# Kernel optimization log

Hardware: AMD Instinct MI355X
Metric: run time of the kernel (lower is better)

## Reference

```python
import jax, jax.numpy as jnp
import numpy as np

DIM = 256
HEADS = 8
PS = 8  # patch/window size
EPS = 1e-5


def _ln(x, g, b):
    m = x.mean(-1, keepdims=True)
    v = x.var(-1, keepdims=True)
    return (x - m) / jnp.sqrt(v + EPS) * g + b


def setup_inputs() -> dict:
    key = jax.random.key(0)
    ks = jax.random.split(key, 10)
    B, C, H, W = 4, DIM, 256, 256
    s = 0.02
    return {
        "y_lf": jax.random.normal(ks[0], (B, C, H, W), jnp.float32),
        "y_hf": jax.random.normal(ks[1], (B, C, H, W), jnp.float32),
        "g_lf": jnp.ones((C,), jnp.float32),
        "b_lf": jnp.zeros((C,), jnp.float32),
        "g_hf": jnp.ones((C,), jnp.float32),
        "b_hf": jnp.zeros((C,), jnp.float32),
        "Wq": jax.random.normal(ks[2], (C, C), jnp.float32) * s,
        "bq": jnp.zeros((C,), jnp.float32),
        "Wk": jax.random.normal(ks[3], (C, C), jnp.float32) * s,
        "bk": jnp.zeros((C,), jnp.float32),
        "Wv": jax.random.normal(ks[4], (C, C), jnp.float32) * s,
        "bv": jnp.zeros((C,), jnp.float32),
        "Wo": jax.random.normal(ks[5], (C, C), jnp.float32) * s,
        "bo": jnp.zeros((C,), jnp.float32),
    }


def reference(y_lf, y_hf, g_lf, b_lf, g_hf, b_hf, Wq, bq, Wk, bk, Wv, bv, Wo, bo):
    B, C, H, W = y_lf.shape
    ps = PS
    hd = C // HEADS
    nH, nW = H // ps, W // ps

    def win_tokens(x):
        # (B,C,H,W) -> (B*nH*nW, ps*ps, C)
        x = x.reshape(B, C, nH, ps, nW, ps)
        return x.transpose(0, 2, 4, 3, 5, 1).reshape(-1, ps * ps, C)

    lf = win_tokens(y_lf)
    hf = win_tokens(y_hf)  # residual + V source (un-normalized, as in torch code)

    q = _ln(lf, g_lf, b_lf) @ Wq.T + bq
    k = _ln(hf, g_hf, b_hf) @ Wk.T + bk
    v = hf @ Wv.T + bv

    BW, L, _ = q.shape
    q = q.reshape(BW, L, HEADS, hd)
    k = k.reshape(BW, L, HEADS, hd)
    v = v.reshape(BW, L, HEADS, hd)

    scale = 1.0 / np.sqrt(hd).astype(np.float32)
    scores = jnp.einsum('bqhd,bkhd->bhqk', q, k) * scale
    attn = jax.nn.softmax(scores, axis=-1)
    o = jnp.einsum('bhqk,bkhd->bqhd', attn, v).reshape(BW, L, C)
    o = o @ Wo.T + bo + hf  # out_proj + residual

    # window_reverse: (B*nH*nW, ps*ps, C) -> (B,C,H,W)
    o = o.reshape(B, nH, nW, ps, ps, C)
    o = o.transpose(0, 5, 1, 3, 2, 4).reshape(B, C, H, W)
    return o
```

## Files before the change

kernel.cpp:

```cpp
#include <hip/hip_runtime.h>

typedef float  f4     __attribute__((ext_vector_type(4)));
typedef float  f32x4  __attribute__((ext_vector_type(4)));
typedef short  short8 __attribute__((ext_vector_type(8)));
typedef __bf16 bf16x8 __attribute__((ext_vector_type(8)));
typedef int    int4v  __attribute__((ext_vector_type(4)));
typedef unsigned short us4 __attribute__((ext_vector_type(4)));

__device__ __forceinline__ unsigned short f2bf(float f) {
    unsigned int u = __builtin_bit_cast(unsigned int, f);
    u += 0x7FFFu + ((u >> 16) & 1u);
    return (unsigned short)(u >> 16);
}
__device__ __forceinline__ float bf2f(unsigned short h) {
    unsigned int u = ((unsigned int)h) << 16;
    return __builtin_bit_cast(float, u);
}
__device__ __forceinline__ f32x4 mfma_bf16(short8 a, short8 b, f32x4 c) {
    return __builtin_amdgcn_mfma_f32_16x16x32_bf16(
        __builtin_bit_cast(bf16x8, a), __builtin_bit_cast(bf16x8, b), c, 0, 0, 0);
}
__device__ __forceinline__ int cvt_pk_bf16(float lo, float hi) {
    int d;
    asm volatile("v_cvt_pk_bf16_f32 %0, %1, %2" : "=v"(d) : "v"(lo), "v"(hi));
    return d;
}
__device__ __forceinline__ int bperm(int addr, int src) {
    return __builtin_amdgcn_ds_bpermute(addr, src);
}

__global__ void pcaf_precvt(const float* __restrict__ Wq, const float* __restrict__ bq,
                            const float* __restrict__ Wk, const float* __restrict__ bk,
                            const float* __restrict__ Wv, const float* __restrict__ Wo,
                            const float* __restrict__ g_lf, const float* __restrict__ b_lf,
                            const float* __restrict__ g_hf, const float* __restrict__ b_hf,
                            void* __restrict__ ws) {
    const int mat  = blockIdx.x >> 8;
    const int row  = blockIdx.x & 255;
    const int lane = threadIdx.x;
    const float* W = (mat == 0) ? Wq : (mat == 1) ? Wk : (mat == 2) ? Wv : Wo;
    f4 w = *(const f4*)(W + row * 256 + lane * 4);
    f4 wp = w;
    if (mat < 2) {
        const float* g = mat ? g_hf : g_lf;
        f4 gg = *(const f4*)(g + lane * 4);
        wp = w * gg;
    }
    us4 u;
    u[0] = f2bf(wp[0]); u[1] = f2bf(wp[1]); u[2] = f2bf(wp[2]); u[3] = f2bf(wp[3]);
    {
        const int ct   = row >> 4;
        const int l15r = row & 15;
        const int k_   = lane >> 3;
        const int g_   = (lane >> 1) & 3;
        const int e4   = (lane & 1) * 4;
        unsigned short* dst = (unsigned short*)ws + mat * 65536 +
                              (((ct * 8 + k_) * 64) + g_ * 16 + l15r) * 8 + e4;
        *(us4*)dst = u;
    }
    if (mat < 2) {
        const float* b = mat ? b_hf : b_lf;
        f4 bb = *(const f4*)(b + lane * 4);
        float rsum = wp[0] + wp[1] + wp[2] + wp[3];
        float cb   = bb[0] * w[0] + bb[1] * w[1] + bb[2] * w[2] + bb[3] * w[3];
        #pragma unroll
        for (int d = 1; d < 64; d <<= 1) {
            rsum += __shfl_xor(rsum, d);
            cb   += __shfl_xor(cb, d);
        }
        if (lane == 0) {
            float* cons = (float*)((char*)ws + 524288);
            cons[mat * 512 + row]       = rsum;
            cons[mat * 512 + 256 + row] = cb + (mat ? bk[row] : bq[row]);
        }
    }
}

constexpr int RS  = 528;
constexpr int HWC = 65536;
constexpr int Wd  = 256;
constexpr int OA  = 0;
constexpr int OB  = 67584;
constexpr int OS  = 135168;

struct AccW { f32x4 a[4][2]; };

__device__ __forceinline__ AccW gemmW(const char* base,
                                      const unsigned short* __restrict__ Wbw,
                                      int lane, int g, int l15) {
    AccW r;
    f32x4 z = {0.f, 0.f, 0.f, 0.f};
    #pragma unroll
    for (int m = 0; m < 4; ++m) { r.a[m][0] = z; r.a[m][1] = z; }
    #pragma unroll
    for (int half = 0; half < 2; ++half) {
        short8 w0[4], w1[4];
        #pragma unroll
        for (int k = 0; k < 4; ++k) {
            w0[k] = *(const short8*)(Wbw + (half * 4 + k) * 512 + lane * 8);
            w1[k] = *(const short8*)(Wbw + 4096 + (half * 4 + k) * 512 + lane * 8);
        }
        #pragma unroll
        for (int k = 0; k < 4; ++k) {
            #pragma unroll
            for (int m = 0; m < 4; ++m) {
                short8 am = *(const short8*)(base + (16 * m + l15) * RS +
                                             ((half * 4 + k) * 32 + g * 8) * 2);
                r.a[m][0] = mfma_bf16(am, w0[k], r.a[m][0]);
                r.a[m][1] = mfma_bf16(am, w1[k], r.a[m][1]);
            }
        }
    }
    return r;
}

__global__ __attribute__((amdgpu_flat_work_group_size(1024, 1024)))
void pcaf8_kernel(
    const float* __restrict__ y_lf, const float* __restrict__ y_hf,
    const float* __restrict__ bv, const float* __restrict__ bo,
    const void* __restrict__ ws, float* __restrict__ out)
{
    __shared__ __align__(16) char sm[137216];

    const unsigned short* wsq = (const unsigned short*)ws;
    const unsigned short* wsk = wsq + 65536;
    const unsigned short* wsv = wsq + 131072;
    const unsigned short* wso = wsq + 196608;
    const float* cons = (const float*)((const char*)ws + 524288);

    const int tid = threadIdx.x;
    const int bid = blockIdx.x;
    const int wi  = ((bid & 7) << 8) | (bid >> 3);
    const int bb  = wi >> 9;
    const int nh  = (wi >> 4) & 31;
    const int nwp = wi & 15;
    const long pair_base = (long)bb * 256 * HWC + (long)(nh * 8) * Wd + nwp * 16;

    const int wave = tid >> 6;
    const int win  = wave >> 3;
    const int head = wave & 7;
    const int lane = tid & 63;
    const int g    = lane >> 4;
    const int l15  = lane & 15;
    const int c0   = 32 * head + l15;
    const int ro   = win * 64;

    {
        f4 lv[8], hv[8];
        #pragma unroll
        for (int it = 0; it < 4; ++it) {
            int q2  = it * 1024 + tid;
            int c2  = q2 >> 5;
            int ph  = (q2 >> 2) & 7;
            int pw4 = (q2 & 3) * 4;
            long go = pair_base + (long)(2 * c2) * HWC + ph * Wd + pw4;
            lv[2 * it]     = *(const f4*)(y_lf + go);
            lv[2 * it + 1] = *(const f4*)(y_lf + go + HWC);
            hv[2 * it]     = *(const f4*)(y_hf + go);
            hv[2 * it + 1] = *(const f4*)(y_hf + go + HWC);
        }
        #pragma unroll
        for (int it = 0; it < 4; ++it) {
            int q2  = it * 1024 + tid;
            int c2  = q2 >> 5;
            int ph  = (q2 >> 2) & 7;
            int pw4 = (q2 & 3) * 4;
            int tok0 = (pw4 >> 3) * 64 + ph * 8 + (pw4 & 7);
            #pragma unroll
            for (int j = 0; j < 4; ++j) {
                unsigned int lvv = (unsigned int)f2bf(lv[2 * it][j]) | ((unsigned int)f2bf(lv[2 * it + 1][j]) << 16);
                unsigned int hvv = (unsigned int)f2bf(hv[2 * it][j]) | ((unsigned int)f2bf(hv[2 * it + 1][j]) << 16);
                *(unsigned int*)(sm + OA + (tok0 + j) * RS + c2 * 4) = lvv;
                *(unsigned int*)(sm + OB + (tok0 + j) * RS + c2 * 4) = hvv;
            }
        }
    }
    __syncthreads();

    {
        const int t = tid >> 3, j = tid & 7;
        #pragma unroll
        for (int pass = 0; pass < 2; ++pass) {
            const int base = pass ? OB : OA;
            float sum = 0.f, ss = 0.f;
            #pragma unroll
            for (int r = 0; r < 4; ++r) {
                short8 raw = *(const short8*)(sm + base + t * RS + (j * 32 + r * 8) * 2);
                #pragma unroll
                for (int e = 0; e < 8; ++e) { float f = bf2f((unsigned short)raw[e]); sum += f; ss += f * f; }
            }
            sum += __shfl_xor(sum, 1); ss += __shfl_xor(ss, 1);
            sum += __shfl_xor(sum, 2); ss += __shfl_xor(ss, 2);
            sum += __shfl_xor(sum, 4); ss += __shfl_xor(ss, 4);
            float mean = sum * (1.f / 256.f);
            float rstd = rsqrtf(ss * (1.f / 256.f) - mean * mean + 1e-5f);
            if (j == 0) {
                float* S = (float*)(sm + OS);
                S[pass * 256 + t]       = mean;
                S[pass * 256 + 128 + t] = rstd;
            }
        }
    }

    AccW qacc = gemmW(sm + OA + ro * RS, wsq + head * 8192, lane, g, l15);

    unsigned int resp[4][2][2];
    #pragma unroll
    for (int m = 0; m < 4; ++m)
        #pragma unroll
        for (int n = 0; n < 2; ++n)
            #pragma unroll
            for (int jh = 0; jh < 2; ++jh) {
                unsigned int lo = *(const unsigned short*)(sm + OB + (ro + 16 * m + 4 * g + 2 * jh) * RS + (c0 + 16 * n) * 2);
                unsigned int hi = *(const unsigned short*)(sm + OB + (ro + 16 * m + 4 * g + 2 * jh + 1) * RS + (c0 + 16 * n) * 2);
                resp[m][n][jh] = lo | (hi << 16);
            }

    int vp[4][2][2];
    {
        AccW vacc = gemmW(sm + OB + ro * RS, wsv + head * 8192, lane, g, l15);
        float bv0 = bv[c0], bv1 = bv[c0 + 16];
        #pragma unroll
        for (int m = 0; m < 4; ++m) {
            vp[m][0][0] = cvt_pk_bf16(vacc.a[m][0][0] + bv0, vacc.a[m][0][1] + bv0);
            vp[m][0][1] = cvt_pk_bf16(vacc.a[m][0][2] + bv0, vacc.a[m][0][3] + bv0);
            vp[m][1][0] = cvt_pk_bf16(vacc.a[m][1][0] + bv1, vacc.a[m][1][1] + bv1);
            vp[m][1][1] = cvt_pk_bf16(vacc.a[m][1][2] + bv1, vacc.a[m][1][3] + bv1);
        }
    }
    __syncthreads();

    {
        const float* S = (const float*)(sm + OS);
        const float SCALE = 0.17677669529663687f;
        float rs0 = cons[c0], rs1 = cons[c0 + 16];
        float cb0 = cons[256 + c0], cb1 = cons[256 + c0 + 16];
        #pragma unroll
        for (int m = 0; m < 4; ++m)
            #pragma unroll
            for (int i = 0; i < 4; ++i) {
                int t = ro + 16 * m + 4 * g + i;
                float mean = S[t], rstd = S[128 + t];
                float v0 = (rstd * (qacc.a[m][0][i] - mean * rs0) + cb0) * SCALE;
                float v1 = (rstd * (qacc.a[m][1][i] - mean * rs1) + cb1) * SCALE;
                *(unsigned short*)(sm + OA + t * RS + c0 * 2)        = f2bf(v0);
                *(unsigned short*)(sm + OA + t * RS + (c0 + 16) * 2) = f2bf(v1);
            }
    }

    AccW kacc = gemmW(sm + OB + ro * RS, wsk + head * 8192, lane, g, l15);
    __syncthreads();

    {
        const float* S = (const float*)(sm + OS);
        float rs0 = cons[512 + c0], rs1 = cons[512 + c0 + 16];
        float cb0 = cons[768 + c0], cb1 = cons[768 + c0 + 16];
        #pragma unroll
        for (int m = 0; m < 4; ++m)
            #pragma unroll
            for (int i = 0; i < 4; ++i) {
                int t = ro + 16 * m + 4 * g + i;
                float mean = S[256 + t], rstd = S[384 + t];
                float v0 = rstd * (kacc.a[m][0][i] - mean * rs0) + cb0;
                float v1 = rstd * (kacc.a[m][1][i] - mean * rs1) + cb1;
                *(unsigned short*)(sm + OB + t * RS + c0 * 2)        = f2bf(v0);
                *(unsigned short*)(sm + OB + t * RS + (c0 + 16) * 2) = f2bf(v1);
            }
    }
    __syncthreads();

    {
        short8 kf[4], qf[4];
        #pragma unroll
        for (int x = 0; x < 4; ++x) {
            kf[x] = *(const short8*)(sm + OB + (ro + 16 * x + l15) * RS + (32 * head + 8 * g) * 2);
            qf[x] = *(const short8*)(sm + OA + (ro + 16 * x + l15) * RS + (32 * head + 8 * g) * 2);
        }
        __syncthreads();

        f32x4 z = {0.f, 0.f, 0.f, 0.f};
        const int a0 = ((2 * (g & 1)) * 16 + l15) * 4;
        const int a1 = a0 + 64;
        const bool ghi = (g >> 1) & 1;

        short8 vf[2][2];
        #pragma unroll
        for (int kk = 0; kk < 2; ++kk)
            #pragma unroll
            for (int n2 = 0; n2 < 2; ++n2) {
                int4v t;
                #pragma unroll
                for (int j = 0; j < 4; ++j) {
                    int ad = (j >> 1) ? a1 : a0;
                    int v0 = bperm(ad, vp[2 * kk][n2][j & 1]);
                    int v1 = bperm(ad, vp[2 * kk + 1][n2][j & 1]);
                    t[j] = ghi ? v1 : v0;
                }
                vf[kk][n2] = __builtin_bit_cast(short8, t);
            }

        f32x4 o[4][2];
        #pragma unroll
        for (int c = 0; c < 4; ++c) { o[c][0] = z; o[c][1] = z; }

        #pragma unroll
        for (int c = 0; c < 4; ++c) {
            f32x4 stc[4];
            #pragma unroll
            for (int nk = 0; nk < 4; ++nk)
                stc[nk] = mfma_bf16(kf[nk], qf[c], z);

            float mx = stc[0][0];
            #pragma unroll
            for (int nk = 0; nk < 4; ++nk)
                #pragma unroll
                for (int i = 0; i < 4; ++i) mx = fmaxf(mx, stc[nk][i]);
            mx = fmaxf(mx, __shfl_xor(mx, 16));
            mx = fmaxf(mx, __shfl_xor(mx, 32));
            float sum = 0.f;
            #pragma unroll
            for (int nk = 0; nk < 4; ++nk)
                #pragma unroll
                for (int i = 0; i < 4; ++i) {
                    float e = __expf(stc[nk][i] - mx);
                    stc[nk][i] = e;
                    sum += e;
                }
            sum += __shfl_xor(sum, 16);
            sum += __shfl_xor(sum, 32);
            float is = 1.f / sum;

            int pq[4][2];
            #pragma unroll
            for (int nk = 0; nk < 4; ++nk) {
                pq[nk][0] = cvt_pk_bf16(stc[nk][0] * is, stc[nk][1] * is);
                pq[nk][1] = cvt_pk_bf16(stc[nk][2] * is, stc[nk][3] * is);
            }

            #pragma unroll
            for (int kk = 0; kk < 2; ++kk) {
                int4v t;
                #pragma unroll
                for (int j = 0; j < 4; ++j) {
                    int ad = (j >> 1) ? a1 : a0;
                    int v0 = bperm(ad, pq[2 * kk][j & 1]);
                    int v1 = bperm(ad, pq[2 * kk + 1][j & 1]);
                    t[j] = ghi ? v1 : v0;
                }
                short8 pf = __builtin_bit_cast(short8, t);
                o[c][0] = mfma_bf16(pf, vf[kk][0], o[c][0]);
                o[c][1] = mfma_bf16(pf, vf[kk][1], o[c][1]);
            }
        }

        #pragma unroll
        for (int c = 0; c < 4; ++c)
            #pragma unroll
            for (int i = 0; i < 4; ++i) {
                int t = ro + 16 * c + 4 * g + i;
                *(unsigned short*)(sm + OA + t * RS + c0 * 2)        = f2bf(o[c][0][i]);
                *(unsigned short*)(sm + OA + t * RS + (c0 + 16) * 2) = f2bf(o[c][1][i]);
            }
    }
    __syncthreads();

    AccW oacc = gemmW(sm + OA + ro * RS, wso + head * 8192, lane, g, l15);
    __syncthreads();

    {
        float bo0 = bo[c0], bo1 = bo[c0 + 16];
        #pragma unroll
        for (int n = 0; n < 2; ++n) {
            float bon = n ? bo1 : bo0;
            int cout = c0 + 16 * n;
            #pragma unroll
            for (int m = 0; m < 4; ++m) {
                int ph  = 2 * m + (g >> 1);
                int pw4 = 4 * (g & 1);
                f4 ov;
                #pragma unroll
                for (int i = 0; i < 4; ++i) {
                    float rv = bf2f((unsigned short)((resp[m][n][i >> 1] >> (16 * (i & 1))) & 0xFFFF));
                    ov[i] = oacc.a[m][n][i] + bon + rv;
                }
                *(f4*)(sm + (cout * 132 + ph * 16 + win * 8 + pw4) * 4) = ov;
            }
        }
    }
    __syncthreads();

    {
        #pragma unroll
        for (int it = 0; it < 8; ++it) {
            int idx = it * 1024 + tid;
            int c   = idx >> 5;
            int rem = idx & 31;
            int ph  = rem >> 2;
            int l4  = rem & 3;
            f4 v = *(const f4*)(sm + (c * 132 + ph * 16 + l4 * 4) * 4);
            *(f4*)(out + pair_base + (long)c * HWC + ph * Wd + l4 * 4) = v;
        }
    }
}

extern "C" void kernel_launch(void* const* d_in, const int* in_sizes, int n_in,
                              void* d_out, int out_size, void* d_ws, size_t ws_size,
                              hipStream_t stream) {
    (void)in_sizes; (void)n_in; (void)out_size; (void)ws_size;
    const float* y_lf = (const float*)d_in[0];
    const float* y_hf = (const float*)d_in[1];
    const float* g_lf = (const float*)d_in[2];
    const float* b_lf = (const float*)d_in[3];
    const float* g_hf = (const float*)d_in[4];
    const float* b_hf = (const float*)d_in[5];
    const float* Wq   = (const float*)d_in[6];
    const float* bq   = (const float*)d_in[7];
    const float* Wk   = (const float*)d_in[8];
    const float* bk   = (const float*)d_in[9];
    const float* Wv   = (const float*)d_in[10];
    const float* bv   = (const float*)d_in[11];
    const float* Wo   = (const float*)d_in[12];
    const float* bo   = (const float*)d_in[13];
    float* out = (float*)d_out;

    pcaf_precvt<<<dim3(1024), dim3(64), 0, stream>>>(
        Wq, bq, Wk, bk, Wv, Wo, g_lf, b_lf, g_hf, b_hf, d_ws);
    pcaf8_kernel<<<dim3(2048), dim3(1024), 0, stream>>>(
        y_lf, y_hf, bv, bo, d_ws, out);
}
```

Before: 508.3 us.

## Compute Q/K transposed in registers and write output directly, dropping LDS round-trips

Q and K projections are now computed with weights as the A operand (transposed accumulators), so the LayerNorm correction and bf16 packing can feed the attention MFMA fragments through lane permutes instead of being stored to and reloaded from shared memory. This removes several barriers and LDS write/read passes. Residual values are read from LDS at output time instead of being held in registers, and the final output is stored straight to global memory without the LDS staging transpose. The per-row LN constants are interleaved for vector loads. The trade-offs are more lane permutes and higher register pressure, plus narrower 16-byte global stores in place of the staged coalesced write pattern.

```diff
diff --git a/kernel.cpp b/kernel.cpp
--- a/kernel.cpp
+++ b/kernel.cpp
@@ -22,7 +22,7 @@
 }
 __device__ __forceinline__ int cvt_pk_bf16(float lo, float hi) {
     int d;
-    asm volatile("v_cvt_pk_bf16_f32 %0, %1, %2" : "=v"(d) : "v"(lo), "v"(hi));
+    asm("v_cvt_pk_bf16_f32 %0, %1, %2" : "=v"(d) : "v"(lo), "v"(hi));
     return d;
 }
 __device__ __forceinline__ int bperm(int addr, int src) {
@@ -70,8 +70,8 @@
         }
         if (lane == 0) {
             float* cons = (float*)((char*)ws + 524288);
-            cons[mat * 512 + row]       = rsum;
-            cons[mat * 512 + 256 + row] = cb + (mat ? bk[row] : bq[row]);
+            cons[mat * 512 + 2 * row]     = rsum;
+            cons[mat * 512 + 2 * row + 1] = cb + (mat ? bk[row] : bq[row]);
         }
     }
 }
@@ -84,6 +84,7 @@
 constexpr int OS  = 135168;
 
 struct AccW { f32x4 a[4][2]; };
+struct AccT { f32x4 a[2][4]; };
 
 __device__ __forceinline__ AccW gemmW(const char* base,
                                       const unsigned short* __restrict__ Wbw,
@@ -114,8 +115,50 @@
     return r;
 }
 
+__device__ __forceinline__ AccT gemmWT(const char* base,
+                                       const unsigned short* __restrict__ Wbw,
+                                       int lane, int g, int l15) {
+    AccT r;
+    f32x4 z = {0.f, 0.f, 0.f, 0.f};
+    #pragma unroll
+    for (int n = 0; n < 4; ++n) { r.a[0][n] = z; r.a[1][n] = z; }
+    #pragma unroll
+    for (int half = 0; half < 2; ++half) {
+        short8 w0[4], w1[4];
+        #pragma unroll
+        for (int k = 0; k < 4; ++k) {
+            w0[k] = *(const short8*)(Wbw + (half * 4 + k) * 512 + lane * 8);
+            w1[k] = *(const short8*)(Wbw + 4096 + (half * 4 + k) * 512 + lane * 8);
+        }
+        #pragma unroll
+        for (int k = 0; k < 4; ++k) {
+            #pragma unroll
+            for (int n = 0; n < 4; ++n) {
+                short8 tk = *(const short8*)(base + (16 * n + l15) * RS +
+                                             ((half * 4 + k) * 32 + g * 8) * 2);
+                r.a[0][n] = mfma_bf16(w0[k], tk, r.a[0][n]);
+                r.a[1][n] = mfma_bf16(w1[k], tk, r.a[1][n]);
+            }
+        }
+    }
+    return r;
+}
+
+__device__ __forceinline__ short8 repack4(const int* p0, const int* p1,
+                                          int a0, int a1, bool ghi) {
+    int4v t;
+    #pragma unroll
+    for (int j = 0; j < 4; ++j) {
+        int ad = (j >> 1) ? a1 : a0;
+        int v0 = bperm(ad, p0[j & 1]);
+        int v1 = bperm(ad, p1[j & 1]);
+        t[j] = ghi ? v1 : v0;
+    }
+    return __builtin_bit_cast(short8, t);
+}
+
 __global__ __attribute__((amdgpu_flat_work_group_size(1024, 1024)))
-void pcaf8_kernel(
+void pcaf12_kernel(
     const float* __restrict__ y_lf, const float* __restrict__ y_hf,
     const float* __restrict__ bv, const float* __restrict__ bo,
     const void* __restrict__ ws, float* __restrict__ out)
@@ -126,7 +169,8 @@
     const unsigned short* wsk = wsq + 65536;
     const unsigned short* wsv = wsq + 131072;
     const unsigned short* wso = wsq + 196608;
-    const float* cons = (const float*)((const char*)ws + 524288);
+    const float* qc = (const float*)((const char*)ws + 524288);
+    const float* kc = qc + 512;
 
     const int tid = threadIdx.x;
     const int bid = blockIdx.x;
@@ -201,25 +245,19 @@
             }
         }
     }
-
-    AccW qacc = gemmW(sm + OA + ro * RS, wsq + head * 8192, lane, g, l15);
-
-    unsigned int resp[4][2][2];
-    #pragma unroll
-    for (int m = 0; m < 4; ++m)
-        #pragma unroll
-        for (int n = 0; n < 2; ++n)
-            #pragma unroll
-            for (int jh = 0; jh < 2; ++jh) {
-                unsigned int lo = *(const unsigned short*)(sm + OB + (ro + 16 * m + 4 * g + 2 * jh) * RS + (c0 + 16 * n) * 2);
-                unsigned int hi = *(const unsigned short*)(sm + OB + (ro + 16 * m + 4 * g + 2 * jh + 1) * RS + (c0 + 16 * n) * 2);
-                resp[m][n][jh] = lo | (hi << 16);
-            }
-
-    int vp[4][2][2];
+    __syncthreads();
+
+    const float* S = (const float*)(sm + OS);
+    const int  a0  = ((2 * (g & 1)) * 16 + l15) * 4;
+    const int  a1  = a0 + 64;
+    const bool ghi = (g >> 1) & 1;
+    f32x4 z = {0.f, 0.f, 0.f, 0.f};
+
+    short8 vf[2][2];
     {
         AccW vacc = gemmW(sm + OB + ro * RS, wsv + head * 8192, lane, g, l15);
         float bv0 = bv[c0], bv1 = bv[c0 + 16];
+        int vp[4][2][2];
         #pragma unroll
         for (int m = 0; m < 4; ++m) {
             vp[m][0][0] = cvt_pk_bf16(vacc.a[m][0][0] + bv0, vacc.a[m][0][1] + bv0);
@@ -227,79 +265,76 @@
             vp[m][1][0] = cvt_pk_bf16(vacc.a[m][1][0] + bv1, vacc.a[m][1][1] + bv1);
             vp[m][1][1] = cvt_pk_bf16(vacc.a[m][1][2] + bv1, vacc.a[m][1][3] + bv1);
         }
-    }
-    __syncthreads();
-
-    {
-        const float* S = (const float*)(sm + OS);
+        #pragma unroll
+        for (int kk = 0; kk < 2; ++kk)
+            #pragma unroll
+            for (int n2 = 0; n2 < 2; ++n2)
+                vf[kk][n2] = repack4(vp[2 * kk][n2], vp[2 * kk + 1][n2], a0, a1, ghi);
+    }
+
+    short8 kf[4];
+    {
+        AccT kacc = gemmWT(sm + OB + ro * RS, wsk + head * 8192, lane, g, l15);
+        float mh[4], rh[4];
+        #pragma unroll
+        for (int n = 0; n < 4; ++n) {
+            mh[n] = S[256 + ro + 16 * n + l15];
+            rh[n] = S[384 + ro + 16 * n + l15];
+        }
+        int kp[2][4][2];
+        #pragma unroll
+        for (int m = 0; m < 2; ++m) {
+            int cb = 32 * head + 16 * m + 4 * g;
+            f4 c0v = *(const f4*)(kc + cb * 2);
+            f4 c1v = *(const f4*)(kc + cb * 2 + 4);
+            #pragma unroll
+            for (int n = 0; n < 4; ++n) {
+                float v0 = rh[n] * (kacc.a[m][n][0] - mh[n] * c0v[0]) + c0v[1];
+                float v1 = rh[n] * (kacc.a[m][n][1] - mh[n] * c0v[2]) + c0v[3];
+                float v2 = rh[n] * (kacc.a[m][n][2] - mh[n] * c1v[0]) + c1v[1];
+                float v3 = rh[n] * (kacc.a[m][n][3] - mh[n] * c1v[2]) + c1v[3];
+                kp[m][n][0] = cvt_pk_bf16(v0, v1);
+                kp[m][n][1] = cvt_pk_bf16(v2, v3);
+            }
+        }
+        #pragma unroll
+        for (int x = 0; x < 4; ++x)
+            kf[x] = repack4(kp[0][x], kp[1][x], a0, a1, ghi);
+    }
+
+    short8 qf[4];
+    {
+        AccT qacc = gemmWT(sm + OA + ro * RS, wsq + head * 8192, lane, g, l15);
         const float SCALE = 0.17677669529663687f;
-        float rs0 = cons[c0], rs1 = cons[c0 + 16];
-        float cb0 = cons[256 + c0], cb1 = cons[256 + c0 + 16];
-        #pragma unroll
-        for (int m = 0; m < 4; ++m)
-            #pragma unroll
-            for (int i = 0; i < 4; ++i) {
-                int t = ro + 16 * m + 4 * g + i;
-                float mean = S[t], rstd = S[128 + t];
-                float v0 = (rstd * (qacc.a[m][0][i] - mean * rs0) + cb0) * SCALE;
-                float v1 = (rstd * (qacc.a[m][1][i] - mean * rs1) + cb1) * SCALE;
-                *(unsigned short*)(sm + OA + t * RS + c0 * 2)        = f2bf(v0);
-                *(unsigned short*)(sm + OA + t * RS + (c0 + 16) * 2) = f2bf(v1);
-            }
-    }
-
-    AccW kacc = gemmW(sm + OB + ro * RS, wsk + head * 8192, lane, g, l15);
-    __syncthreads();
-
-    {
-        const float* S = (const float*)(sm + OS);
-        float rs0 = cons[512 + c0], rs1 = cons[512 + c0 + 16];
-        float cb0 = cons[768 + c0], cb1 = cons[768 + c0 + 16];
-        #pragma unroll
-        for (int m = 0; m < 4; ++m)
-            #pragma unroll
-            for (int i = 0; i < 4; ++i) {
-                int t = ro + 16 * m + 4 * g + i;
-                float mean = S[256 + t], rstd = S[384 + t];
-                float v0 = rstd * (kacc.a[m][0][i] - mean * rs0) + cb0;
-                float v1 = rstd * (kacc.a[m][1][i] - mean * rs1) + cb1;
-                *(unsigned short*)(sm + OB + t * RS + c0 * 2)        = f2bf(v0);
-                *(unsigned short*)(sm + OB + t * RS + (c0 + 16) * 2) = f2bf(v1);
-            }
-    }
-    __syncthreads();
-
-    {
-        short8 kf[4], qf[4];
-        #pragma unroll
-        for (int x = 0; x < 4; ++x) {
-            kf[x] = *(const short8*)(sm + OB + (ro + 16 * x + l15) * RS + (32 * head + 8 * g) * 2);
-            qf[x] = *(const short8*)(sm + OA + (ro + 16 * x + l15) * RS + (32 * head + 8 * g) * 2);
-        }
-        __syncthreads();
-
-        f32x4 z = {0.f, 0.f, 0.f, 0.f};
-        const int a0 = ((2 * (g & 1)) * 16 + l15) * 4;
-        const int a1 = a0 + 64;
-        const bool ghi = (g >> 1) & 1;
-
-        short8 vf[2][2];
-        #pragma unroll
-        for (int kk = 0; kk < 2; ++kk)
-            #pragma unroll
-            for (int n2 = 0; n2 < 2; ++n2) {
-                int4v t;
-                #pragma unroll
-                for (int j = 0; j < 4; ++j) {
-                    int ad = (j >> 1) ? a1 : a0;
-                    int v0 = bperm(ad, vp[2 * kk][n2][j & 1]);
-                    int v1 = bperm(ad, vp[2 * kk + 1][n2][j & 1]);
-                    t[j] = ghi ? v1 : v0;
-                }
-                vf[kk][n2] = __builtin_bit_cast(short8, t);
-            }
-
-        f32x4 o[4][2];
+        float ml[4], rl[4];
+        #pragma unroll
+        for (int n = 0; n < 4; ++n) {
+            ml[n] = S[ro + 16 * n + l15];
+            rl[n] = S[128 + ro + 16 * n + l15];
+        }
+        int qp[2][4][2];
+        #pragma unroll
+        for (int m = 0; m < 2; ++m) {
+            int cb = 32 * head + 16 * m + 4 * g;
+            f4 c0v = *(const f4*)(qc + cb * 2);
+            f4 c1v = *(const f4*)(qc + cb * 2 + 4);
+            #pragma unroll
+            for (int n = 0; n < 4; ++n) {
+                float v0 = (rl[n] * (qacc.a[m][n][0] - ml[n] * c0v[0]) + c0v[1]) * SCALE;
+                float v1 = (rl[n] * (qacc.a[m][n][1] - ml[n] * c0v[2]) + c0v[3]) * SCALE;
+                float v2 = (rl[n] * (qacc.a[m][n][2] - ml[n] * c1v[0]) + c1v[1]) * SCALE;
+                float v3 = (rl[n] * (qacc.a[m][n][3] - ml[n] * c1v[2]) + c1v[3]) * SCALE;
+                qp[m][n][0] = cvt_pk_bf16(v0, v1);
+                qp[m][n][1] = cvt_pk_bf16(v2, v3);
+            }
+        }
+        #pragma unroll
+        for (int x = 0; x < 4; ++x)
+            qf[x] = repack4(qp[0][x], qp[1][x], a0, a1, ghi);
+    }
+
+    f32x4 o[4][2];
+    {
         #pragma unroll
         for (int c = 0; c < 4; ++c) { o[c][0] = z; o[c][1] = z; }
 
@@ -339,35 +374,27 @@
 
             #pragma unroll
             for (int kk = 0; kk < 2; ++kk) {
-                int4v t;
-                #pragma unroll
-                for (int j = 0; j < 4; ++j) {
-                    int ad = (j >> 1) ? a1 : a0;
-                    int v0 = bperm(ad, pq[2 * kk][j & 1]);
-                    int v1 = bperm(ad, pq[2 * kk + 1][j & 1]);
-                    t[j] = ghi ? v1 : v0;
-                }
-                short8 pf = __builtin_bit_cast(short8, t);
+                short8 pf = repack4(pq[2 * kk], pq[2 * kk + 1], a0, a1, ghi);
                 o[c][0] = mfma_bf16(pf, vf[kk][0], o[c][0]);
                 o[c][1] = mfma_bf16(pf, vf[kk][1], o[c][1]);
             }
         }
-
-        #pragma unroll
-        for (int c = 0; c < 4; ++c)
-            #pragma unroll
-            for (int i = 0; i < 4; ++i) {
-                int t = ro + 16 * c + 4 * g + i;
-                *(unsigned short*)(sm + OA + t * RS + c0 * 2)        = f2bf(o[c][0][i]);
-                *(unsigned short*)(sm + OA + t * RS + (c0 + 16) * 2) = f2bf(o[c][1][i]);
-            }
     }
     __syncthreads();
 
-    AccW oacc = gemmW(sm + OA + ro * RS, wso + head * 8192, lane, g, l15);
+    #pragma unroll
+    for (int c = 0; c < 4; ++c)
+        #pragma unroll
+        for (int i = 0; i < 4; ++i) {
+            int t = ro + 16 * c + 4 * g + i;
+            *(unsigned short*)(sm + OA + t * RS + c0 * 2)        = f2bf(o[c][0][i]);
+            *(unsigned short*)(sm + OA + t * RS + (c0 + 16) * 2) = f2bf(o[c][1][i]);
+        }
     __syncthreads();
 
     {
+        AccW oacc = gemmW(sm + OA + ro * RS, wso + head * 8192, lane, g, l15);
+        const long win_base = pair_base + win * 8;
         float bo0 = bo[c0], bo1 = bo[c0 + 16];
         #pragma unroll
         for (int n = 0; n < 2; ++n) {
@@ -375,30 +402,17 @@
             int cout = c0 + 16 * n;
             #pragma unroll
             for (int m = 0; m < 4; ++m) {
-                int ph  = 2 * m + (g >> 1);
-                int pw4 = 4 * (g & 1);
+                int tok0 = 16 * m + 4 * g;
+                int ph = tok0 >> 3, pw = tok0 & 7;
                 f4 ov;
                 #pragma unroll
                 for (int i = 0; i < 4; ++i) {
-                    float rv = bf2f((unsigned short)((resp[m][n][i >> 1] >> (16 * (i & 1))) & 0xFFFF));
+                    float rv = bf2f(*(const unsigned short*)(
+                        sm + OB + (ro + tok0 + i) * RS + cout * 2));
                     ov[i] = oacc.a[m][n][i] + bon + rv;
                 }
-                *(f4*)(sm + (cout * 132 + ph * 16 + win * 8 + pw4) * 4) = ov;
-            }
-        }
-    }
-    __syncthreads();
-
-    {
-        #pragma unroll
-        for (int it = 0; it < 8; ++it) {
-            int idx = it * 1024 + tid;
-            int c   = idx >> 5;
-            int rem = idx & 31;
-            int ph  = rem >> 2;
-            int l4  = rem & 3;
-            f4 v = *(const f4*)(sm + (c * 132 + ph * 16 + l4 * 4) * 4);
-            *(f4*)(out + pair_base + (long)c * HWC + ph * Wd + l4 * 4) = v;
+                *(f4*)(out + win_base + (long)cout * HWC + ph * Wd + pw) = ov;
+            }
         }
     }
 }
@@ -425,6 +439,6 @@
 
     pcaf_precvt<<<dim3(1024), dim3(64), 0, stream>>>(
         Wq, bq, Wk, bk, Wv, Wo, g_lf, b_lf, g_hf, b_hf, d_ws);
-    pcaf8_kernel<<<dim3(2048), dim3(1024), 0, stream>>>(
+    pcaf12_kernel<<<dim3(2048), dim3(1024), 0, stream>>>(
         y_lf, y_hf, bv, bo, d_ws, out);
 }
```

After: 545.9 us. +7.4%, slower.
